# Kernel tuning notes

Measured on AMD Instinct MI355X. Metric: run time of the kernel, lower is better.

## Reference

```python
import jax, jax.numpy as jnp
from jax import lax
import numpy as np

# Module config (from init_kwargs)
NUM_SEG_ROW = 8
NUM_SEG_COL = 8
H = 224
W = 224
K = NUM_SEG_ROW * NUM_SEG_COL  # 64 labels
B = 4


def setup_inputs() -> dict:
    key = jax.random.key(0)
    grad_map = jax.random.normal(key, (B, 1, H, W), dtype=jnp.float32)
    return {"grad_map": grad_map, "band_width": 5, "num_iterations": 5}


def _dp_paths(neg_g):
    """Dynamic-programming min-cost path. neg_g: (L, P, M) per-step costs.
    Returns positions (L, P): index in [0, M) chosen at each step."""
    L, P, M = neg_g.shape
    m = jnp.arange(M)
    # clamp(m + {-1,0,1}, 0, M-1); torch's inf padding is never hit after clamping
    nbr = jnp.clip(m[:, None] + jnp.array([-1, 0, 1])[None, :], 0, M - 1)  # (M,3)

    def step(prev_cost, g_row):
        pc = prev_cost[:, nbr]                      # (P, M, 3)
        amin = pc.argmin(axis=2)                    # (P, M)
        min_prev = jnp.take_along_axis(pc, amin[..., None], axis=2)[..., 0]
        path_row = nbr[m[None, :], amin]            # (P, M) predecessor position
        new_cost = min_prev + g_row
        return new_cost, (new_cost, path_row)

    _, (costs, paths) = lax.scan(step, neg_g[0], neg_g[1:])  # paths: (L-1, P, M)
    idx_last = costs[-1].argmin(axis=1)             # (P,)

    def back(idx, path_row):
        new_idx = path_row[jnp.arange(path_row.shape[0]), idx]
        return new_idx, idx

    first_idx, pos_tail = lax.scan(back, idx_last, paths, reverse=True)
    positions = jnp.concatenate([first_idx[None], pos_tail], axis=0)  # (L, P)
    return positions


def _boundary_masks(grad2d, x_inits, y_inits, band_width):
    """grad2d: (H, W). Returns (vmask, hmask) boolean (H, W)."""
    offs = jnp.arange(-band_width, band_width + 1)
    P = x_inits.shape[0]
    # vertical paths (one x per row)
    x_idx = jnp.clip(x_inits[:, None] + offs[None, :], 0, W - 1)   # (P, M)
    pos_v = _dp_paths(-grad2d[:, x_idx])                            # (H, P)
    coords_v = x_idx[jnp.arange(P)[None, :], pos_v]                 # (H, P) x-coords
    vmask = jnp.zeros((H, W), bool).at[jnp.arange(H)[:, None], coords_v].set(True)
    # horizontal paths (one y per column)
    y_idx = jnp.clip(y_inits[:, None] + offs[None, :], 0, H - 1)    # (P, M)
    pos_h = _dp_paths(-grad2d.T[:, y_idx])                          # (W, P)
    coords_h = y_idx[jnp.arange(P)[None, :], pos_h]                 # (W, P) y-coords
    hmask = jnp.zeros((H, W), bool).at[coords_h, jnp.arange(W)[:, None]].set(True)
    return vmask, hmask


def _one_hot_nchw(labels):
    return jax.nn.one_hot(labels, K, dtype=jnp.float32).transpose(0, 3, 1, 2)


def _box_vote(oh, ksize):
    # grouped (depthwise) conv with all-ones kernel == neighborhood vote count
    kern = jnp.ones((K, 1, ksize, ksize), oh.dtype)
    pad = ksize // 2
    return lax.conv_general_dilated(
        oh, kern, window_strides=(1, 1), padding=[(pad, pad), (pad, pad)],
        dimension_numbers=("NCHW", "OIHW", "NCHW"), feature_group_count=K)


def reference(grad_map, band_width, num_iterations):
    x_inits = jnp.clip(jnp.array([i * (W // NUM_SEG_COL) for i in range(1, NUM_SEG_COL)]), 0, W - 1)
    y_inits = jnp.clip(jnp.array([i * (H // NUM_SEG_ROW) for i in range(1, NUM_SEG_ROW)]), 0, H - 1)
    vmask, hmask = jax.vmap(lambda g: _boundary_masks(g, x_inits, y_inits, band_width))(grad_map[:, 0])
    v_labels = jnp.cumsum(vmask.astype(jnp.int32), axis=2)
    h_labels = jnp.cumsum(hmask.astype(jnp.int32), axis=1)
    seg = v_labels + NUM_SEG_COL * h_labels                         # (B, H, W), values in [0, K)
    # multi-scale connectivity voting
    oh = _one_hot_nchw(seg)
    labels = seg
    for _ in range(num_iterations):
        vote_sum = _box_vote(oh, 3) + _box_vote(oh, 5) + _box_vote(oh, 7)
        labels = vote_sum.argmax(axis=1)
        oh = _one_hot_nchw(labels)
    return labels
```

## Files before the change

### kernel.cpp

```cpp
#include <hip/hip_runtime.h>
#include <stdint.h>

#define HH 224
#define WW 224
#define BB 4
#define PP 7
#define SEG 28
#define BW 5
#define MM 11

#define POS_INF_I 0x7F800000

typedef const __attribute__((address_space(1))) unsigned int* gas_ptr;
typedef __attribute__((address_space(3))) unsigned int* las_ptr;
typedef unsigned long long ull;

__device__ inline ull mcompose(ull F, ull G) {
    ull H = 0ull;
#pragma unroll
    for (int i = 0; i < 11; ++i) {
        unsigned g = (unsigned)(G >> (4 * i)) & 15u;
        H |= ((F >> (4 * g)) & 15ull) << (4 * i);
    }
    return H;
}

__global__ __launch_bounds__(64) void dp_kernel(const float* __restrict__ grad,
                                                int* __restrict__ coords_v,
                                                int* __restrict__ coords_h) {
    __shared__ __align__(16) float gseg[225 * 16];

    const int tid = threadIdx.x;
    const int l   = tid & 15;
    const int sid = blockIdx.x;
    const int p   = sid % PP;
    const int dir = (sid / PP) & 1;
    const int b   = sid / (2 * PP);
    const int base = SEG * (p + 1);
    const float* gb = grad + b * (HH * WW);

    {
        const int r  = tid >> 4;
        const int m  = tid & 15;
        const int sS = (dir == 0) ? WW : 1;
        const int sM = (dir == 0) ? 1  : WW;
        const float* src = gb + r * sS + (base - BW + m) * sM;
        const long stepBytes = (long)(4 * sS) * 4;
#pragma unroll 8
        for (int c = 0; c < 56; ++c) {
            __builtin_amdgcn_global_load_lds((gas_ptr)(const void*)src,
                                             (las_ptr)(void*)(&gseg[c * 64]), 4, 0, 0);
            src = (const float*)((const char*)src + stepBytes);
        }
    }
    __syncthreads();

    const float lane_add = (l < MM) ? 0.0f : __int_as_float(POS_INF_I);
    const float* gp = &gseg[l];

    unsigned wreg[16] = {};

#define DP_STEP(gval, ownb, jj_c)                                                       \
    {                                                                                   \
        float v1 = cost;                                                                \
        float v0 = __int_as_float(__builtin_amdgcn_update_dpp(                          \
            POS_INF_I, __float_as_int(cost), 0x111, 0xf, 0xf, false));                  \
        float v2 = __int_as_float(__builtin_amdgcn_update_dpp(                          \
            POS_INF_I, __float_as_int(cost), 0x101, 0xf, 0xf, false));                  \
        bool a01 = (v0 <= v1), a02 = (v0 <= v2), a12 = (v1 <= v2);                      \
        bool aa  = a01 && a02;                                                          \
        unsigned long long A   = __ballot(aa);                                          \
        unsigned long long C12 = __ballot(a12);                                         \
        unsigned long long B0 = ~A & C12;                                               \
        unsigned long long B1 = ~A & ~C12;                                              \
        float mv = aa ? v0 : (a12 ? v1 : v2);                                           \
        cost = mv - (gval) + lane_add;                                                  \
        unsigned wv = (unsigned)(B0 & 0x7FFull) | ((unsigned)(B1 & 0x7FFull) << 11);    \
        wreg[(jj_c)] = (ownb) ? wv : wreg[(jj_c)];                                      \
    }

    float cost = -gp[0] + lane_add;
    float buf[16], c0[16];
#pragma unroll
    for (int k = 0; k < 16; ++k) buf[k] = gp[(1 + k) * 16];
    for (int t = 0; t < 13; ++t) {
        const bool own = (tid == t);
#pragma unroll
        for (int k = 0; k < 16; ++k) c0[k] = buf[k];
#pragma unroll
        for (int k = 0; k < 16; ++k) buf[k] = gp[(16 * (t + 1) + 1 + k) * 16];
#pragma unroll
        for (int k = 0; k < 16; ++k) DP_STEP(c0[k], own, k)
    }
    {
        const bool own = (tid == 13);
#pragma unroll
        for (int k = 0; k < 15; ++k) DP_STEP(buf[k], own, k)
    }
#undef DP_STEP

    float bc = cost;
    int   bi = l;
#pragma unroll
    for (int mask = 1; mask < 16; mask <<= 1) {
        float oc = __shfl_xor(bc, mask, 16);
        int   oi = __shfl_xor(bi, mask, 16);
        if (oc < bc || (oc == bc && oi < bi)) { bc = oc; bi = oi; }
    }
    const int idx_last = bi;

    const int mcnt = (l < 13) ? 16 : ((l == 13) ? 15 : 0);
    const ull IDMAP = 0xA9876543210ull;
    ull L = IDMAP;
#pragma unroll
    for (int jj = 15; jj >= 0; --jj) {
        if (jj < mcnt) {
            unsigned ww = wreg[jj];
            ull M = 0ull;
#pragma unroll
            for (int i = 0; i < MM; ++i) {
                unsigned sel = ((ww >> i) & 1u) + 2u * ((ww >> (11 + i)) & 1u);
                M |= ((ull)(i + (int)sel - 1)) << (4 * i);
            }
            L = mcompose(M, L);
        }
    }
    ull I = L;
#pragma unroll
    for (int d = 1; d < 16; d <<= 1) {
        ull O = __shfl_down(I, d, 16);
        if (l + d < 16) I = mcompose(I, O);
    }
    ull R = __shfl_down(I, 1, 16);
    if (l == 15) R = IDMAP;

    int* cout = (dir == 0) ? coords_v : coords_h;
    if (tid == 15) cout[(b * HH + 223) * PP + p] = base + idx_last - BW;
    if (tid < 16) {
        unsigned v = (unsigned)(R >> (4 * idx_last)) & 15u;
#pragma unroll
        for (int jj = 15; jj >= 0; --jj) {
            if (jj < mcnt) {
                unsigned ww = wreg[jj];
                unsigned sel = ((ww >> v) & 1u) + 2u * ((ww >> (11 + v)) & 1u);
                v = v + sel - 1u;
                cout[(b * HH + (16 * l + jj)) * PP + p] = base + (int)v - BW;
            }
        }
    }
}

#define RW 38
#define RH 14
#define RSTR 40

__global__ __launch_bounds__(256) void labvote_kernel(const int* __restrict__ cv,
                                                      const int* __restrict__ ch,
                                                      unsigned char* __restrict__ out8) {
    __shared__ unsigned char lab[RH * RSTR];
    __shared__ unsigned bins[16 * 256];
    const int tx = threadIdx.x, ty = threadIdx.y;
    const int t  = ty * 32 + tx;
    const int b  = blockIdx.z;
    const int GX0 = blockIdx.x * 32, GY0 = blockIdx.y * 8;

    for (int idx = t; idx < RW * RH; idx += 256) {
        int j = idx / RW, i = idx - j * RW;
        int gx = GX0 - 3 + i, gy = GY0 - 3 + j;
        if ((unsigned)gx < WW && (unsigned)gy < HH) {
            const int* cvp = cv + (b * HH + gy) * PP;
            const int* chp = ch + (b * WW + gx) * PP;
            int v = 0, h = 0;
#pragma unroll
            for (int q = 0; q < PP; ++q) { v += (cvp[q] <= gx); h += (chp[q] <= gy); }
            lab[j * RSTR + i] = (unsigned char)(v + 8 * h);
        }
    }
    __syncthreads();

    const int gx = GX0 + tx, gy = GY0 + ty;
#pragma unroll
    for (int c = 0; c < 16; ++c) bins[c * 256 + t] = 0u;
#pragma unroll
    for (int dy = -3; dy <= 3; ++dy) {
        if ((unsigned)(gy + dy) >= HH) continue;
#pragma unroll
        for (int dx = -3; dx <= 3; ++dx) {
            if ((unsigned)(gx + dx) >= WW) continue;
            int lb = lab[(ty + 3 + dy) * RSTR + (tx + 3 + dx)];
            int ay = dy < 0 ? -dy : dy, ax = dx < 0 ? -dx : dx;
            int d = ay > ax ? ay : ax;
            unsigned wgt = (d <= 1) ? 3u : (unsigned)(4 - d);
            atomicAdd(&bins[(lb >> 2) * 256 + t], wgt << ((lb & 3) * 8));
        }
    }
    int best_s = 0, best_k = 0;
#pragma unroll
    for (int c = 0; c < 16; ++c) {
        unsigned wd = bins[c * 256 + t];
        if (wd) {
#pragma unroll
            for (int q = 0; q < 4; ++q) {
                int s = (int)((wd >> (q * 8)) & 255u);
                if (s > best_s) { best_s = s; best_k = c * 4 + q; }
            }
        }
    }
    out8[(b * HH + gy) * WW + gx] = (unsigned char)best_k;
}

__global__ __launch_bounds__(256) void vote_kernel(const unsigned char* __restrict__ in,
                                                   unsigned char* __restrict__ out8,
                                                   int* __restrict__ out32) {
    __shared__ unsigned bins[16 * 256];
    const int tx = threadIdx.x, ty = threadIdx.y;
    const int t  = ty * 32 + tx;
    const int x  = blockIdx.x * 32 + tx;
    const int y  = blockIdx.y * 8 + ty;
    const int b  = blockIdx.z;
    const unsigned char* img = in + b * (HH * WW);

    ull rows[7];
    const bool xedge = (blockIdx.x == 0) || (blockIdx.x == (WW / 32 - 1));
    if (!xedge) {
        const unsigned* img32 = (const unsigned*)img;
        const int o0 = x - 3;
#pragma unroll
        for (int dy = -3; dy <= 3; ++dy) {
            int yc = min(max(y + dy, 0), HH - 1);
            int o  = yc * WW + o0;
            int a  = o >> 2;
            int sh = (o & 3) * 8;
            unsigned d0 = img32[a], d1 = img32[a + 1], d2 = img32[a + 2];
            ull lo = ((ull)d1 << 32) | d0;
            ull row = lo >> sh;
            if (sh) row |= (ull)d2 << (64 - sh);
            rows[dy + 3] = row & 0x00FFFFFFFFFFFFFFull;
        }
    } else {
#pragma unroll
        for (int dy = -3; dy <= 3; ++dy) {
            int yc = min(max(y + dy, 0), HH - 1);
            ull row = 0ull;
#pragma unroll
            for (int dx = -3; dx <= 3; ++dx) {
                int xc = min(max(x + dx, 0), WW - 1);
                row |= (ull)img[yc * WW + xc] << (8 * (dx + 3));
            }
            rows[dy + 3] = row;
        }
    }

    const unsigned labc = (unsigned)((rows[3] >> 24) & 255u);
    const ull rep = (ull)labc * 0x0001010101010101ull;
    bool uni = true;
#pragma unroll
    for (int k = 0; k < 7; ++k) uni = uni && (rows[k] == rep);

    int best_k;
    if (uni) {
        best_k = (int)labc;
    } else {
#pragma unroll
        for (int c = 0; c < 16; ++c) bins[c * 256 + t] = 0u;
#pragma unroll
        for (int dy = -3; dy <= 3; ++dy) {
            if ((unsigned)(y + dy) >= (unsigned)HH) continue;
            ull row = rows[dy + 3];
            const int ay = dy < 0 ? -dy : dy;
#pragma unroll
            for (int dx = -3; dx <= 3; ++dx) {
                if ((unsigned)(x + dx) >= (unsigned)WW) continue;
                int lb = (int)((row >> (8 * (dx + 3))) & 255u);
                const int ax = dx < 0 ? -dx : dx;
                const int d = ay > ax ? ay : ax;
                const unsigned wgt = (d <= 1) ? 3u : (unsigned)(4 - d);
                atomicAdd(&bins[(lb >> 2) * 256 + t], wgt << ((lb & 3) * 8));
            }
        }
        int best_s = 0; best_k = 0;
#pragma unroll
        for (int c = 0; c < 16; ++c) {
            unsigned wd = bins[c * 256 + t];
            if (wd) {
#pragma unroll
                for (int q = 0; q < 4; ++q) {
                    int s = (int)((wd >> (q * 8)) & 255u);
                    if (s > best_s) { best_s = s; best_k = c * 4 + q; }
                }
            }
        }
    }

    int o = (b * HH + y) * WW + x;
    if (out8)  out8[o]  = (unsigned char)best_k;
    if (out32) out32[o] = best_k;
}

extern "C" void kernel_launch(void* const* d_in, const int* in_sizes, int n_in,
                              void* d_out, int out_size, void* d_ws, size_t ws_size,
                              hipStream_t stream) {
    const float* grad = (const float*)d_in[0];
    int* out = (int*)d_out;
    char* ws = (char*)d_ws;

    int* cv = (int*)(ws);
    int* ch = (int*)(ws + 25088);
    unsigned char* laW = (unsigned char*)(ws + 50176);
    unsigned char* laD = (unsigned char*)d_out;

    dp_kernel<<<56, 64, 0, stream>>>(grad, cv, ch);

    dim3 grid(WW / 32, HH / 8, BB), blk(32, 8, 1);
    labvote_kernel<<<grid, blk, 0, stream>>>(cv, ch, laD);
    vote_kernel<<<grid, blk, 0, stream>>>(laD, laW, nullptr);
    vote_kernel<<<grid, blk, 0, stream>>>(laW, laD, nullptr);
    vote_kernel<<<grid, blk, 0, stream>>>(laD, laW, nullptr);
    vote_kernel<<<grid, blk, 0, stream>>>(laW, nullptr, out);
}
```

Measured before the change: 119.5 us.

## Fuse label build and five vote iterations into one halo-tiled kernel

Replaces the label kernel and four separate vote launches with a single kernel. Each block computes labels for a 62x38 region with a 15-pixel halo in shared memory, then runs all five vote passes in LDS with shrinking margins, ping-ponging between two buffers. Out-of-image pixels are marked 255 and skipped, and the shared-memory atomics become plain adds because each thread owns its own bins. This removes four launches and the global round-trips of intermediate labels, at the cost of redundant halo computation and more shared memory per block.

```diff
diff --git a/kernel.cpp b/kernel.cpp
--- a/kernel.cpp
+++ b/kernel.cpp
@@ -10,6 +10,10 @@
 #define MM 11
 
 #define POS_INF_I 0x7F800000
+
+#define RGW 62
+#define RGH 38
+#define RSTRIDE 64
 
 typedef const __attribute__((address_space(1))) unsigned int* gas_ptr;
 typedef __attribute__((address_space(3))) unsigned int* las_ptr;
@@ -150,48 +154,23 @@
     }
 }
 
-#define RW 38
-#define RH 14
-#define RSTR 40
-
-__global__ __launch_bounds__(256) void labvote_kernel(const int* __restrict__ cv,
-                                                      const int* __restrict__ ch,
-                                                      unsigned char* __restrict__ out8) {
-    __shared__ unsigned char lab[RH * RSTR];
-    __shared__ unsigned bins[16 * 256];
-    const int tx = threadIdx.x, ty = threadIdx.y;
-    const int t  = ty * 32 + tx;
-    const int b  = blockIdx.z;
-    const int GX0 = blockIdx.x * 32, GY0 = blockIdx.y * 8;
-
-    for (int idx = t; idx < RW * RH; idx += 256) {
-        int j = idx / RW, i = idx - j * RW;
-        int gx = GX0 - 3 + i, gy = GY0 - 3 + j;
-        if ((unsigned)gx < WW && (unsigned)gy < HH) {
-            const int* cvp = cv + (b * HH + gy) * PP;
-            const int* chp = ch + (b * WW + gx) * PP;
-            int v = 0, h = 0;
-#pragma unroll
-            for (int q = 0; q < PP; ++q) { v += (cvp[q] <= gx); h += (chp[q] <= gy); }
-            lab[j * RSTR + i] = (unsigned char)(v + 8 * h);
-        }
-    }
-    __syncthreads();
-
-    const int gx = GX0 + tx, gy = GY0 + ty;
+
+__device__ __forceinline__ int slow_vote(const ull* rows, int t, unsigned* bins) {
 #pragma unroll
     for (int c = 0; c < 16; ++c) bins[c * 256 + t] = 0u;
 #pragma unroll
-    for (int dy = -3; dy <= 3; ++dy) {
-        if ((unsigned)(gy + dy) >= HH) continue;
-#pragma unroll
-        for (int dx = -3; dx <= 3; ++dx) {
-            if ((unsigned)(gx + dx) >= WW) continue;
-            int lb = lab[(ty + 3 + dy) * RSTR + (tx + 3 + dx)];
-            int ay = dy < 0 ? -dy : dy, ax = dx < 0 ? -dx : dx;
-            int d = ay > ax ? ay : ax;
-            unsigned wgt = (d <= 1) ? 3u : (unsigned)(4 - d);
-            atomicAdd(&bins[(lb >> 2) * 256 + t], wgt << ((lb & 3) * 8));
+    for (int dy = 0; dy < 7; ++dy) {
+        ull row = rows[dy];
+        const int ay = dy < 3 ? 3 - dy : dy - 3;
+#pragma unroll
+        for (int dx = 0; dx < 7; ++dx) {
+            unsigned lb = (unsigned)((row >> (8 * dx)) & 255u);
+            if (lb != 255u) {
+                const int ax = dx < 3 ? 3 - dx : dx - 3;
+                const int d = ay > ax ? ay : ax;
+                const unsigned wgt = (d <= 1) ? 3u : (unsigned)(4 - d);
+                bins[(lb >> 2) * 256 + t] += wgt << ((lb & 3) * 8);
+            }
         }
     }
     int best_s = 0, best_k = 0;
@@ -206,115 +185,127 @@
             }
         }
     }
-    out8[(b * HH + gy) * WW + gx] = (unsigned char)best_k;
-}
-
-__global__ __launch_bounds__(256) void vote_kernel(const unsigned char* __restrict__ in,
-                                                   unsigned char* __restrict__ out8,
+    return best_k;
+}
+
+__device__ __forceinline__ void gather_rows(const unsigned char* src, int px, int py,
+                                            ull* rows) {
+#pragma unroll
+    for (int dy = 0; dy < 7; ++dy) {
+        int o  = (py + dy - 3) * RSTRIDE + (px - 3);
+        int a8 = o & ~7;
+        int sh = (o & 7) * 8;
+        ull lo = *reinterpret_cast<const ull*>(src + a8);
+        ull hi = *reinterpret_cast<const ull*>(src + a8 + 8);
+        ull row = lo >> sh;
+        if (sh) row |= hi << (64 - sh);
+        rows[dy] = row & 0x00FFFFFFFFFFFFFFull;
+    }
+}
+
+template<int MARG>
+__device__ __forceinline__ void vote_iter(const unsigned char* src, unsigned char* dst,
+                                          int t, unsigned* bins) {
+    constexpr int WK = RGW - 2 * MARG;
+    constexpr int HK = RGH - 2 * MARG;
+    for (int idx = t; idx < WK * HK; idx += 256) {
+        int py = MARG + idx / WK;
+        int px = MARG + idx - (idx / WK) * WK;
+        int center = py * RSTRIDE + px;
+        unsigned cl = src[center];
+        unsigned char res;
+        if (cl == 255u) {
+            res = 255;
+        } else {
+            ull rows[7];
+            gather_rows(src, px, py, rows);
+            const ull rep = (ull)cl * 0x0001010101010101ull;
+            bool uni = true;
+#pragma unroll
+            for (int k = 0; k < 7; ++k) uni = uni && (rows[k] == rep);
+            res = uni ? (unsigned char)cl : (unsigned char)slow_vote(rows, t, bins);
+        }
+        dst[center] = res;
+    }
+}
+
+__global__ __launch_bounds__(256) void mega_kernel(const int* __restrict__ cv,
+                                                   const int* __restrict__ ch,
                                                    int* __restrict__ out32) {
-    __shared__ unsigned bins[16 * 256];
-    const int tx = threadIdx.x, ty = threadIdx.y;
-    const int t  = ty * 32 + tx;
-    const int x  = blockIdx.x * 32 + tx;
-    const int y  = blockIdx.y * 8 + ty;
+    __shared__ __align__(16) unsigned bins[16 * 256];
+    __shared__ __align__(16) unsigned char labA[RGH * RSTRIDE];
+    __shared__ __align__(16) unsigned char labB[RGH * RSTRIDE];
+    __shared__ int cvs[RGH * PP];
+    __shared__ int chs[RGW * PP];
+
+    const int t  = threadIdx.x;
     const int b  = blockIdx.z;
-    const unsigned char* img = in + b * (HH * WW);
-
-    ull rows[7];
-    const bool xedge = (blockIdx.x == 0) || (blockIdx.x == (WW / 32 - 1));
-    if (!xedge) {
-        const unsigned* img32 = (const unsigned*)img;
-        const int o0 = x - 3;
-#pragma unroll
-        for (int dy = -3; dy <= 3; ++dy) {
-            int yc = min(max(y + dy, 0), HH - 1);
-            int o  = yc * WW + o0;
-            int a  = o >> 2;
-            int sh = (o & 3) * 8;
-            unsigned d0 = img32[a], d1 = img32[a + 1], d2 = img32[a + 2];
-            ull lo = ((ull)d1 << 32) | d0;
-            ull row = lo >> sh;
-            if (sh) row |= (ull)d2 << (64 - sh);
-            rows[dy + 3] = row & 0x00FFFFFFFFFFFFFFull;
-        }
-    } else {
-#pragma unroll
-        for (int dy = -3; dy <= 3; ++dy) {
-            int yc = min(max(y + dy, 0), HH - 1);
-            ull row = 0ull;
-#pragma unroll
-            for (int dx = -3; dx <= 3; ++dx) {
-                int xc = min(max(x + dx, 0), WW - 1);
-                row |= (ull)img[yc * WW + xc] << (8 * (dx + 3));
-            }
-            rows[dy + 3] = row;
-        }
-    }
-
-    const unsigned labc = (unsigned)((rows[3] >> 24) & 255u);
-    const ull rep = (ull)labc * 0x0001010101010101ull;
-    bool uni = true;
-#pragma unroll
-    for (int k = 0; k < 7; ++k) uni = uni && (rows[k] == rep);
-
-    int best_k;
-    if (uni) {
-        best_k = (int)labc;
-    } else {
-#pragma unroll
-        for (int c = 0; c < 16; ++c) bins[c * 256 + t] = 0u;
-#pragma unroll
-        for (int dy = -3; dy <= 3; ++dy) {
-            if ((unsigned)(y + dy) >= (unsigned)HH) continue;
-            ull row = rows[dy + 3];
-            const int ay = dy < 0 ? -dy : dy;
-#pragma unroll
-            for (int dx = -3; dx <= 3; ++dx) {
-                if ((unsigned)(x + dx) >= (unsigned)WW) continue;
-                int lb = (int)((row >> (8 * (dx + 3))) & 255u);
-                const int ax = dx < 0 ? -dx : dx;
-                const int d = ay > ax ? ay : ax;
-                const unsigned wgt = (d <= 1) ? 3u : (unsigned)(4 - d);
-                atomicAdd(&bins[(lb >> 2) * 256 + t], wgt << ((lb & 3) * 8));
-            }
-        }
-        int best_s = 0; best_k = 0;
-#pragma unroll
-        for (int c = 0; c < 16; ++c) {
-            unsigned wd = bins[c * 256 + t];
-            if (wd) {
-#pragma unroll
-                for (int q = 0; q < 4; ++q) {
-                    int s = (int)((wd >> (q * 8)) & 255u);
-                    if (s > best_s) { best_s = s; best_k = c * 4 + q; }
-                }
-            }
-        }
-    }
-
-    int o = (b * HH + y) * WW + x;
-    if (out8)  out8[o]  = (unsigned char)best_k;
-    if (out32) out32[o] = best_k;
+    const int ox = blockIdx.x * 32 - 15;
+    const int oy = blockIdx.y * 8 - 15;
+
+    for (int idx = t; idx < RGH * PP; idx += 256) {
+        int gy = oy + idx / PP;
+        cvs[idx] = ((unsigned)gy < HH) ? cv[(b * HH + gy) * PP + idx % PP] : 0x7fffffff;
+    }
+    for (int idx = t; idx < RGW * PP; idx += 256) {
+        int gx = ox + idx / PP;
+        chs[idx] = ((unsigned)gx < WW) ? ch[(b * WW + gx) * PP + idx % PP] : 0x7fffffff;
+    }
+    __syncthreads();
+
+    for (int idx = t; idx < RGW * RGH; idx += 256) {
+        int py = idx / RGW;
+        int px = idx - py * RGW;
+        int gx = ox + px, gy = oy + py;
+        unsigned char lbl = 255;
+        if ((unsigned)gx < WW && (unsigned)gy < HH) {
+            int v = 0, h = 0;
+#pragma unroll
+            for (int q = 0; q < PP; ++q) {
+                v += (cvs[py * PP + q] <= gx);
+                h += (chs[px * PP + q] <= gy);
+            }
+            lbl = (unsigned char)(v + 8 * h);
+        }
+        labA[py * RSTRIDE + px] = lbl;
+    }
+    __syncthreads();
+
+    vote_iter<3>(labA, labB, t, bins);  __syncthreads();
+    vote_iter<6>(labB, labA, t, bins);  __syncthreads();
+    vote_iter<9>(labA, labB, t, bins);  __syncthreads();
+    vote_iter<12>(labB, labA, t, bins); __syncthreads();
+
+    {
+        const int px = 15 + (t & 31);
+        const int py = 15 + (t >> 5);
+        unsigned cl = labA[py * RSTRIDE + px];
+        int res;
+        ull rows[7];
+        gather_rows(labA, px, py, rows);
+        const ull rep = (ull)cl * 0x0001010101010101ull;
+        bool uni = true;
+#pragma unroll
+        for (int k = 0; k < 7; ++k) uni = uni && (rows[k] == rep);
+        res = uni ? (int)cl : slow_vote(rows, t, bins);
+        const int gx = ox + px, gy = oy + py;
+        out32[(b * HH + gy) * WW + gx] = res;
+    }
 }
 
 extern "C" void kernel_launch(void* const* d_in, const int* in_sizes, int n_in,
                               void* d_out, int out_size, void* d_ws, size_t ws_size,
                               hipStream_t stream) {
+    (void)in_sizes; (void)n_in; (void)out_size; (void)ws_size;
     const float* grad = (const float*)d_in[0];
     int* out = (int*)d_out;
     char* ws = (char*)d_ws;
 
     int* cv = (int*)(ws);
     int* ch = (int*)(ws + 25088);
-    unsigned char* laW = (unsigned char*)(ws + 50176);
-    unsigned char* laD = (unsigned char*)d_out;
 
     dp_kernel<<<56, 64, 0, stream>>>(grad, cv, ch);
 
-    dim3 grid(WW / 32, HH / 8, BB), blk(32, 8, 1);
-    labvote_kernel<<<grid, blk, 0, stream>>>(cv, ch, laD);
-    vote_kernel<<<grid, blk, 0, stream>>>(laD, laW, nullptr);
-    vote_kernel<<<grid, blk, 0, stream>>>(laW, laD, nullptr);
-    vote_kernel<<<grid, blk, 0, stream>>>(laD, laW, nullptr);
-    vote_kernel<<<grid, blk, 0, stream>>>(laW, nullptr, out);
-}
+    dim3 grid(WW / 32, HH / 8, BB), blk(256, 1, 1);
+    mega_kernel<<<grid, blk, 0, stream>>>(cv, ch, out);
+}
```

After: 185.8 us. 55.5% more time.
